# Performance work log

Measured on AMD Instinct MI355X. Metric: run time of the kernel, lower is better.

## Reference

```python
import jax, jax.numpy as jnp
import numpy as np

N_NODES = 200000
N_CLUSTERS = 50000
D_FEAT = 256


def _segment_mean(vals, seg_ids, num_segments):
    # sum per segment, divide by counts (guard empty segments)
    sums = jax.ops.segment_sum(vals, seg_ids, num_segments=num_segments)
    counts = jax.ops.segment_sum(jnp.ones((vals.shape[0],), vals.dtype), seg_ids,
                                 num_segments=num_segments)
    return sums / jnp.maximum(counts, 1.0)[:, None]


def setup_inputs() -> dict:
    key = jax.random.key(0)
    k1, k2, k3, k4, k5 = jax.random.split(key, 5)
    x = jax.random.normal(k1, (N_NODES, D_FEAT), dtype=jnp.float32)
    h = jax.random.normal(k2, (N_NODES, D_FEAT), dtype=jnp.float32)
    pos = jax.random.normal(k3, (N_NODES, 3), dtype=jnp.float32)
    cluster_map = jax.random.randint(k4, (N_NODES,), 0, N_CLUSTERS, dtype=jnp.int32)
    sample_index = jax.random.randint(k5, (N_CLUSTERS,), 0, N_NODES, dtype=jnp.int32)
    return {"x": x, "h": h, "pos": pos, "cluster_map": cluster_map,
            "sample_index": sample_index, "num_clusters": N_CLUSTERS}


def reference(x, h, pos, cluster_map, sample_index, num_clusters):
    # scatter(x, cluster_map, dim=0, reduce='mean')
    x_pooled = _segment_mean(x, cluster_map, num_clusters)   # [C, D]
    # scatter(h, cluster_map, dim=0, reduce='mean')
    h_pooled = _segment_mean(h, cluster_map, num_clusters)   # [C, D]
    # pos = pos[sample_index]
    pos_sampled = pos[sample_index]                          # [C, 3]
    return (x_pooled, h_pooled, pos_sampled)
```

## Files before the change

kernel.cpp:

```cpp
#include <hip/hip_runtime.h>

#define DF 256

typedef float f32x4 __attribute__((ext_vector_type(4)));

__global__ void cp_count(const int* __restrict__ cmap, int* __restrict__ counts, int n) {
    int i = blockIdx.x * blockDim.x + threadIdx.x;
    if (i < n) atomicAdd(&counts[cmap[i]], 1);
}

__global__ void cp_scanA(const int* __restrict__ counts, int* __restrict__ offsets,
                         int* __restrict__ blocksums, int C) {
    __shared__ int s[256];
    int tid = threadIdx.x;
    int i = blockIdx.x * 256 + tid;
    int v = (i < C) ? counts[i] : 0;
    s[tid] = v;
    __syncthreads();
    for (int off = 1; off < 256; off <<= 1) {
        int t = (tid >= off) ? s[tid - off] : 0;
        __syncthreads();
        s[tid] += t;
        __syncthreads();
    }
    if (i < C) offsets[i] = s[tid] - v;
    if (tid == 255) blocksums[blockIdx.x] = s[255];
}

__global__ void cp_scanB(int* __restrict__ blocksums, int nb) {
    __shared__ int s[256];
    int tid = threadIdx.x;
    if (nb <= 256) {
        int v = (tid < nb) ? blocksums[tid] : 0;
        s[tid] = v;
        __syncthreads();
        for (int off = 1; off < 256; off <<= 1) {
            int t = (tid >= off) ? s[tid - off] : 0;
            __syncthreads();
            s[tid] += t;
            __syncthreads();
        }
        if (tid < nb) blocksums[tid] = s[tid] - v;
    } else if (tid == 0) {
        int run = 0;
        for (int k = 0; k < nb; ++k) { int t = blocksums[k]; blocksums[k] = run; run += t; }
    }
}

__global__ void cp_scanC(int* __restrict__ offsets, const int* __restrict__ blocksums,
                         const int* __restrict__ counts, int2* __restrict__ seg, int C) {
    int i = blockIdx.x * 256 + threadIdx.x;
    if (i < C) {
        int st = offsets[i] + blocksums[blockIdx.x];
        offsets[i] = st;
        seg[i] = make_int2(st, counts[i]);
    }
}

__global__ void cp_fill(const int* __restrict__ cmap, const int* __restrict__ offsets,
                        int* __restrict__ cursor, int* __restrict__ node_list, int n) {
    int i = blockIdx.x * blockDim.x + threadIdx.x;
    if (i < n) {
        int c = cmap[i];
        int slot = atomicAdd(&cursor[c], 1);
        node_list[offsets[c] + slot] = i;
    }
}

__global__ void cp_pool(const float* __restrict__ x, const float* __restrict__ h,
                        const int2* __restrict__ seg, const int* __restrict__ node_list,
                        float* __restrict__ xp, float* __restrict__ hp, int C) {
    int c = blockIdx.x * 4 + (threadIdx.x >> 6);
    if (c >= C) return;
    int lane = threadIdx.x & 63;
    int2 sl = seg[c];
    int start = sl.x, len = sl.y;

    int nid = 0;
    if (lane < len) nid = node_list[start + lane];

    f32x4 ax = 0.f;
    f32x4 ah = 0.f;
    int kmax = len < 64 ? len : 64;
    int k = 0;
    for (; k + 4 <= kmax; k += 4) {
        int n0 = __shfl(nid, k);
        int n1 = __shfl(nid, k + 1);
        int n2 = __shfl(nid, k + 2);
        int n3 = __shfl(nid, k + 3);
        f32x4 x0 = reinterpret_cast<const f32x4*>(x + (size_t)n0 * DF)[lane];
        f32x4 h0 = __builtin_nontemporal_load(reinterpret_cast<const f32x4*>(h + (size_t)n0 * DF) + lane);
        f32x4 x1 = reinterpret_cast<const f32x4*>(x + (size_t)n1 * DF)[lane];
        f32x4 h1 = __builtin_nontemporal_load(reinterpret_cast<const f32x4*>(h + (size_t)n1 * DF) + lane);
        f32x4 x2 = reinterpret_cast<const f32x4*>(x + (size_t)n2 * DF)[lane];
        f32x4 h2 = __builtin_nontemporal_load(reinterpret_cast<const f32x4*>(h + (size_t)n2 * DF) + lane);
        f32x4 x3 = reinterpret_cast<const f32x4*>(x + (size_t)n3 * DF)[lane];
        f32x4 h3 = __builtin_nontemporal_load(reinterpret_cast<const f32x4*>(h + (size_t)n3 * DF) + lane);
        ax += x0 + x1 + x2 + x3;
        ah += h0 + h1 + h2 + h3;
    }
    for (; k < kmax; ++k) {
        int n0 = __shfl(nid, k);
        ax += reinterpret_cast<const f32x4*>(x + (size_t)n0 * DF)[lane];
        ah += __builtin_nontemporal_load(reinterpret_cast<const f32x4*>(h + (size_t)n0 * DF) + lane);
    }
    for (int kk = 64; kk < len; ++kk) {
        int n0 = node_list[start + kk];
        ax += reinterpret_cast<const f32x4*>(x + (size_t)n0 * DF)[lane];
        ah += __builtin_nontemporal_load(reinterpret_cast<const f32x4*>(h + (size_t)n0 * DF) + lane);
    }

    float inv = 1.0f / (float)(len > 0 ? len : 1);
    f32x4 vx = ax * inv;
    f32x4 vh = ah * inv;
    __builtin_nontemporal_store(vx, reinterpret_cast<f32x4*>(xp + (size_t)c * DF) + lane);
    __builtin_nontemporal_store(vh, reinterpret_cast<f32x4*>(hp + (size_t)c * DF) + lane);
}

__global__ void cp_pos(const float* __restrict__ pos, const int* __restrict__ sidx,
                       float* __restrict__ out, int C) {
    int i = blockIdx.x * blockDim.x + threadIdx.x;
    if (i >= C) return;
    int s = sidx[i];
    float p0 = pos[(size_t)s * 3 + 0];
    float p1 = pos[(size_t)s * 3 + 1];
    float p2 = pos[(size_t)s * 3 + 2];
    __builtin_nontemporal_store(p0, &out[(size_t)i * 3 + 0]);
    __builtin_nontemporal_store(p1, &out[(size_t)i * 3 + 1]);
    __builtin_nontemporal_store(p2, &out[(size_t)i * 3 + 2]);
}

extern "C" void kernel_launch(void* const* d_in, const int* in_sizes, int n_in,
                              void* d_out, int out_size, void* d_ws, size_t ws_size,
                              hipStream_t stream) {
    const float* x    = (const float*)d_in[0];
    const float* h    = (const float*)d_in[1];
    const float* pos  = (const float*)d_in[2];
    const int*   cmap = (const int*)d_in[3];
    const int*   sidx = (const int*)d_in[4];

    const int n_nodes = in_sizes[2] / 3;
    const int C       = in_sizes[4];

    float* out  = (float*)d_out;
    float* xp   = out;
    float* hp   = out + (size_t)C * DF;
    float* pout = out + (size_t)2 * C * DF;

    int*  counts    = (int*)d_ws;
    int*  cursor    = counts + C;
    int*  offsets   = cursor + C;
    int*  blocksums = offsets + C;
    int2* seg       = (int2*)(blocksums + 256);
    int*  node_list = (int*)(seg + C);

    hipMemsetAsync(counts, 0, (size_t)2 * C * sizeof(int), stream);

    cp_count<<<(n_nodes + 255) / 256, 256, 0, stream>>>(cmap, counts, n_nodes);

    int nb = (C + 255) / 256;
    cp_scanA<<<nb, 256, 0, stream>>>(counts, offsets, blocksums, C);
    cp_scanB<<<1, 256, 0, stream>>>(blocksums, nb);
    cp_scanC<<<nb, 256, 0, stream>>>(offsets, blocksums, counts, seg, C);

    cp_fill<<<(n_nodes + 255) / 256, 256, 0, stream>>>(cmap, offsets, cursor, node_list, n_nodes);

    cp_pool<<<(C + 3) / 4, 256, 0, stream>>>(x, h, seg, node_list, xp, hp, C);

    cp_pos<<<(C + 255) / 256, 256, 0, stream>>>(pos, sidx, pout, C);
}
```

Measured before the change: 114.6 us.

## Replace three-pass scan with atomic-tail block scan and fuse pos gather into pool

The three-kernel prefix scan becomes a single kernel in which each block reserves its base offset with an atomic add on a global tail counter. It writes absolute start positions straight into the cursor, so the fill kernel no longer reads a separate offsets array. The pos gather is folded into the pool kernel as extra blocks, removing another launch. Segments are no longer laid out in cluster order, which is fine because pool reads each segment's start and length from seg. The intent is to cut kernel launch and inter-kernel gaps, which matter at this runtime.

```diff
diff --git a/kernel.cpp b/kernel.cpp
--- a/kernel.cpp
+++ b/kernel.cpp
@@ -9,9 +9,10 @@
     if (i < n) atomicAdd(&counts[cmap[i]], 1);
 }
 
-__global__ void cp_scanA(const int* __restrict__ counts, int* __restrict__ offsets,
-                         int* __restrict__ blocksums, int C) {
+__global__ void cp_scan(const int* __restrict__ counts, int* __restrict__ tail,
+                        int2* __restrict__ seg, int* __restrict__ cursor, int C) {
     __shared__ int s[256];
+    __shared__ int base;
     int tid = threadIdx.x;
     int i = blockIdx.x * 256 + tid;
     int v = (i < C) ? counts[i] : 0;
@@ -23,53 +24,44 @@
         s[tid] += t;
         __syncthreads();
     }
-    if (i < C) offsets[i] = s[tid] - v;
-    if (tid == 255) blocksums[blockIdx.x] = s[255];
-}
-
-__global__ void cp_scanB(int* __restrict__ blocksums, int nb) {
-    __shared__ int s[256];
-    int tid = threadIdx.x;
-    if (nb <= 256) {
-        int v = (tid < nb) ? blocksums[tid] : 0;
-        s[tid] = v;
-        __syncthreads();
-        for (int off = 1; off < 256; off <<= 1) {
-            int t = (tid >= off) ? s[tid - off] : 0;
-            __syncthreads();
-            s[tid] += t;
-            __syncthreads();
-        }
-        if (tid < nb) blocksums[tid] = s[tid] - v;
-    } else if (tid == 0) {
-        int run = 0;
-        for (int k = 0; k < nb; ++k) { int t = blocksums[k]; blocksums[k] = run; run += t; }
+    if (tid == 255) base = atomicAdd(tail, s[255]);
+    __syncthreads();
+    if (i < C) {
+        int st = base + s[tid] - v;
+        cursor[i] = st;
+        seg[i] = make_int2(st, v);
     }
 }
 
-__global__ void cp_scanC(int* __restrict__ offsets, const int* __restrict__ blocksums,
-                         const int* __restrict__ counts, int2* __restrict__ seg, int C) {
-    int i = blockIdx.x * 256 + threadIdx.x;
-    if (i < C) {
-        int st = offsets[i] + blocksums[blockIdx.x];
-        offsets[i] = st;
-        seg[i] = make_int2(st, counts[i]);
-    }
-}
-
-__global__ void cp_fill(const int* __restrict__ cmap, const int* __restrict__ offsets,
-                        int* __restrict__ cursor, int* __restrict__ node_list, int n) {
+__global__ void cp_fill(const int* __restrict__ cmap, int* __restrict__ cursor,
+                        int* __restrict__ node_list, int n) {
     int i = blockIdx.x * blockDim.x + threadIdx.x;
     if (i < n) {
-        int c = cmap[i];
-        int slot = atomicAdd(&cursor[c], 1);
-        node_list[offsets[c] + slot] = i;
+        int pos = atomicAdd(&cursor[cmap[i]], 1);
+        node_list[pos] = i;
     }
 }
 
 __global__ void cp_pool(const float* __restrict__ x, const float* __restrict__ h,
                         const int2* __restrict__ seg, const int* __restrict__ node_list,
-                        float* __restrict__ xp, float* __restrict__ hp, int C) {
+                        float* __restrict__ xp, float* __restrict__ hp, int C,
+                        int poolBlocks,
+                        const float* __restrict__ pos, const int* __restrict__ sidx,
+                        float* __restrict__ pout) {
+    if (blockIdx.x >= poolBlocks) {
+        int i = (blockIdx.x - poolBlocks) * blockDim.x + threadIdx.x;
+        if (i < C) {
+            int s = sidx[i];
+            float p0 = pos[(size_t)s * 3 + 0];
+            float p1 = pos[(size_t)s * 3 + 1];
+            float p2 = pos[(size_t)s * 3 + 2];
+            __builtin_nontemporal_store(p0, &pout[(size_t)i * 3 + 0]);
+            __builtin_nontemporal_store(p1, &pout[(size_t)i * 3 + 1]);
+            __builtin_nontemporal_store(p2, &pout[(size_t)i * 3 + 2]);
+        }
+        return;
+    }
+
     int c = blockIdx.x * 4 + (threadIdx.x >> 6);
     if (c >= C) return;
     int lane = threadIdx.x & 63;
@@ -117,19 +109,6 @@
     __builtin_nontemporal_store(vh, reinterpret_cast<f32x4*>(hp + (size_t)c * DF) + lane);
 }
 
-__global__ void cp_pos(const float* __restrict__ pos, const int* __restrict__ sidx,
-                       float* __restrict__ out, int C) {
-    int i = blockIdx.x * blockDim.x + threadIdx.x;
-    if (i >= C) return;
-    int s = sidx[i];
-    float p0 = pos[(size_t)s * 3 + 0];
-    float p1 = pos[(size_t)s * 3 + 1];
-    float p2 = pos[(size_t)s * 3 + 2];
-    __builtin_nontemporal_store(p0, &out[(size_t)i * 3 + 0]);
-    __builtin_nontemporal_store(p1, &out[(size_t)i * 3 + 1]);
-    __builtin_nontemporal_store(p2, &out[(size_t)i * 3 + 2]);
-}
-
 extern "C" void kernel_launch(void* const* d_in, const int* in_sizes, int n_in,
                               void* d_out, int out_size, void* d_ws, size_t ws_size,
                               hipStream_t stream) {
@@ -148,24 +127,22 @@
     float* pout = out + (size_t)2 * C * DF;
 
     int*  counts    = (int*)d_ws;
-    int*  cursor    = counts + C;
-    int*  offsets   = cursor + C;
-    int*  blocksums = offsets + C;
-    int2* seg       = (int2*)(blocksums + 256);
+    int*  tail      = counts + C;
+    int*  cursor    = tail + 1;
+    int2* seg       = (int2*)(cursor + C);
     int*  node_list = (int*)(seg + C);
 
-    hipMemsetAsync(counts, 0, (size_t)2 * C * sizeof(int), stream);
+    hipMemsetAsync(counts, 0, (size_t)(C + 1) * sizeof(int), stream);
 
     cp_count<<<(n_nodes + 255) / 256, 256, 0, stream>>>(cmap, counts, n_nodes);
 
     int nb = (C + 255) / 256;
-    cp_scanA<<<nb, 256, 0, stream>>>(counts, offsets, blocksums, C);
-    cp_scanB<<<1, 256, 0, stream>>>(blocksums, nb);
-    cp_scanC<<<nb, 256, 0, stream>>>(offsets, blocksums, counts, seg, C);
+    cp_scan<<<nb, 256, 0, stream>>>(counts, tail, seg, cursor, C);
 
-    cp_fill<<<(n_nodes + 255) / 256, 256, 0, stream>>>(cmap, offsets, cursor, node_list, n_nodes);
+    cp_fill<<<(n_nodes + 255) / 256, 256, 0, stream>>>(cmap, cursor, node_list, n_nodes);
 
-    cp_pool<<<(C + 3) / 4, 256, 0, stream>>>(x, h, seg, node_list, xp, hp, C);
-
-    cp_pos<<<(C + 255) / 256, 256, 0, stream>>>(pos, sidx, pout, C);
+    int poolBlocks = (C + 3) / 4;
+    int posBlocks  = (C + 255) / 256;
+    cp_pool<<<poolBlocks + posBlocks, 256, 0, stream>>>(
+        x, h, seg, node_list, xp, hp, C, poolBlocks, pos, sidx, pout);
 }
```

Result: no change. 112.5 us (-1.8%).
